# Performance work log

Measured on AMD Instinct MI355X. Metric: run time of the kernel, lower is better.

Reference implementation:

```python
import jax, jax.numpy as jnp
import numpy as np

B, S, H = 4, 2048, 1024
NH, HD = 16, 64
FF = 4096
EPS = 1e-5

def _ln(x, g, b):
    m = jnp.mean(x, axis=-1, keepdims=True)
    v = jnp.var(x, axis=-1, keepdims=True)
    return (x - m) * jax.lax.rsqrt(v + EPS) * g + b

def setup_inputs() -> dict:
    key = jax.random.key(0)
    ks = jax.random.split(key, 12)
    sc = 0.02
    return {
        "hidden_states": jax.random.normal(ks[0], (B, S, H), jnp.float32),
        "Wq": jax.random.normal(ks[1], (H, H), jnp.float32) * sc,
        "bq": jnp.zeros((H,), jnp.float32),
        "Wk": jax.random.normal(ks[2], (H, H), jnp.float32) * sc,
        "bk": jnp.zeros((H,), jnp.float32),
        "Wv": jax.random.normal(ks[3], (H, H), jnp.float32) * sc,
        "bv": jnp.zeros((H,), jnp.float32),
        "Wi": jax.random.normal(ks[4], (H, FF), jnp.float32) * sc,
        "bi": jnp.zeros((FF,), jnp.float32),
        "Wo": jax.random.normal(ks[5], (FF, H), jnp.float32) * sc,
        "bo": jnp.zeros((H,), jnp.float32),
        "g1": jnp.ones((H,), jnp.float32),
        "b1": jnp.zeros((H,), jnp.float32),
        "g2": jnp.ones((H,), jnp.float32),
        "b2": jnp.zeros((H,), jnp.float32),
    }

def reference(hidden_states, Wq, bq, Wk, bk, Wv, bv, Wi, bi, Wo, bo, g1, b1, g2, b2):
    x = hidden_states
    # projections -> [B, NH, S, HD]
    def split(t):
        return t.reshape(B, S, NH, HD).transpose(0, 2, 1, 3)
    q = split(x @ Wq + bq)
    k = split(x @ Wk + bk)
    v = split(x @ Wv + bv)
    scores = jnp.einsum('bhqd,bhkd->bhqk', q, k) / jnp.sqrt(jnp.float32(HD))
    probs = jax.nn.softmax(scores, axis=-1)
    ctx = jnp.einsum('bhqk,bhkd->bhqd', probs, v)
    attn_out = ctx.transpose(0, 2, 1, 3).reshape(B, S, H)
    h = _ln(x + attn_out, g1, b1)
    ffn = jax.nn.gelu(h @ Wi + bi, approximate=False) @ Wo + bo
    return _ln(h + ffn, g2, b2)
```

## Files before the change

kernel.cpp:

```cpp
#include <hip/hip_runtime.h>

#define B_  4
#define S_  2048
#define H_  1024
#define NH_ 16
#define HD_ 64
#define FF_ 4096
#define M_  (B_*S_)

typedef __bf16 bf16x8 __attribute__((ext_vector_type(8)));
typedef float  f32x4  __attribute__((ext_vector_type(4)));
typedef unsigned short ushort8v __attribute__((ext_vector_type(8)));
typedef unsigned short ushort4v __attribute__((ext_vector_type(4)));

typedef __attribute__((address_space(1))) void GVOID;
typedef __attribute__((address_space(3))) void LVOID;

__device__ __forceinline__ void g2l16(const void* g, void* l) {
  __builtin_amdgcn_global_load_lds((GVOID*)g, (LVOID*)l, 16, 0, 0);
}

#define MFMA16(a, b, c) __builtin_amdgcn_mfma_f32_16x16x32_bf16(a, b, c, 0, 0, 0)

#if __has_builtin(__builtin_amdgcn_exp2f)
#define EXP2(x) __builtin_amdgcn_exp2f(x)
#else
#define EXP2(x) exp2f(x)
#endif

__device__ __forceinline__ unsigned short f2bf(float f) {
  unsigned int u = __float_as_uint(f);
  u += 0x7fffu + ((u >> 16) & 1u);
  return (unsigned short)(u >> 16);
}
__device__ __forceinline__ float bf2f(unsigned short h) {
  return __uint_as_float(((unsigned int)h) << 16);
}

__device__ __forceinline__ float gelu_fast(float v) {
  float y = 0.7978845608f * (v + 0.044715f * v * v * v);
  float e = EXP2(y * 2.8853900818f);
  float th = 1.0f - 2.0f / (e + 1.0f);
  return 0.5f * v * (1.0f + th);
}

__device__ __forceinline__ void xcd_swz(int& bx, int& by) {
  int gx = gridDim.x;
  int flat = by * gx + bx;
  int cpx = (gx * gridDim.y) >> 3;
  int swz = (flat & 7) * cpx + (flat >> 3);
  bx = swz % gx;
  by = swz / gx;
}

__device__ __forceinline__ void xcd_swzT(int& bx, int& by) {
  int gy = gridDim.y;
  int flat = bx * gy + by;
  int cpx = (gridDim.x * gy) >> 3;
  int swz = (flat & 7) * cpx + (flat >> 3);
  by = swz % gy;
  bx = swz / gy;
}

__global__ __launch_bounds__(256) void cast_f32_bf16(const float* __restrict__ in,
                                                     unsigned short* __restrict__ out,
                                                     int n4) {
  int i = blockIdx.x * 256 + threadIdx.x;
  if (i >= n4) return;
  float4 v = reinterpret_cast<const float4*>(in)[i];
  ushort4v o;
  o[0] = f2bf(v.x); o[1] = f2bf(v.y); o[2] = f2bf(v.z); o[3] = f2bf(v.w);
  reinterpret_cast<ushort4v*>(out)[i] = o;
}

__global__ __launch_bounds__(256) void prep_weights(const float* __restrict__ Wq,
                                                    const float* __restrict__ Wk,
                                                    const float* __restrict__ Wv,
                                                    const float* __restrict__ Wi,
                                                    const float* __restrict__ Wo,
                                                    unsigned short* __restrict__ WqkvT,
                                                    unsigned short* __restrict__ WiT,
                                                    unsigned short* __restrict__ WoT) {
  __shared__ float t[32][33];
  int id = blockIdx.x;
  const float* in; unsigned short* out; int R, C, bx, by;
  if (id < 3072) {
    int seg = id >> 10, rem = id & 1023;
    in = (seg == 0) ? Wq : (seg == 1) ? Wk : Wv;
    out = WqkvT + (size_t)seg * H_ * H_;
    R = H_; C = H_;
    bx = rem & 31; by = rem >> 5;
  } else if (id < 3072 + 4096) {
    int rem = id - 3072;
    in = Wi; out = WiT; R = H_; C = FF_;
    bx = rem & 127; by = rem >> 7;
  } else {
    int rem = id - 3072 - 4096;
    in = Wo; out = WoT; R = FF_; C = H_;
    bx = rem & 31; by = rem >> 5;
  }
  bx *= 32; by *= 32;
  const int tx = threadIdx.x & 31, ty = threadIdx.x >> 5;
#pragma unroll
  for (int i = 0; i < 32; i += 8)
    t[ty + i][tx] = in[(size_t)(by + ty + i) * C + bx + tx];
  __syncthreads();
#pragma unroll
  for (int i = 0; i < 32; i += 8)
    out[(size_t)(bx + ty + i) * R + by + tx] = f2bf(t[tx][ty + i]);
}

#define ALOAD(bufv, mf, ks)                                                      \
  *reinterpret_cast<const bf16x8*>((char*)As + (bufv)*32768 + wm*16384 +         \
      ((mf)*16 + lr)*128 + (((((ks)*4 + kg)) ^ (lr & 7)) * 16))
#define BLOAD(bufv, nf, ks)                                                      \
  *reinterpret_cast<const bf16x8*>((char*)Bs + (bufv)*32768 + bh*16384 +         \
      (brow0 + (nf)*16 + lr)*128 + (((((ks)*4 + kg)) ^ (lr & 7)) * 16))

#define W4 asm volatile("s_waitcnt vmcnt(4)" ::: "memory")
#define W0 asm volatile("s_waitcnt vmcnt(0)" ::: "memory")
#define WN ((void)0)

#define PH_MFMA(MF0)                                                             \
  __builtin_amdgcn_s_barrier();                                                  \
  asm volatile("s_waitcnt lgkmcnt(0)" ::: "memory");                             \
  __builtin_amdgcn_s_setprio(1);                                                 \
  _Pragma("unroll")                                                              \
  for (int nf = 0; nf < 4; ++nf) {                                               \
    acc[MF0][nf]     = MFMA16(a_[0][0], bfr[nf][0], acc[MF0][nf]);               \
    acc[MF0][nf]     = MFMA16(a_[0][1], bfr[nf][1], acc[MF0][nf]);               \
    acc[MF0 + 1][nf] = MFMA16(a_[1][0], bfr[nf][0], acc[MF0 + 1][nf]);           \
    acc[MF0 + 1][nf] = MFMA16(a_[1][1], bfr[nf][1], acc[MF0 + 1][nf]);           \
  }                                                                              \
  __builtin_amdgcn_s_setprio(0);

#define GEMM_TILE(bufL, STGA, STGB, WAITOP)                                      \
  {                                                                              \
    bf16x8 bfr[4][2];                                                            \
    bf16x8 a_[2][2];                                                             \
    _Pragma("unroll")                                                            \
    for (int nf = 0; nf < 4; ++nf) {                                             \
      bfr[nf][0] = BLOAD(bufL, nf, 0);                                           \
      bfr[nf][1] = BLOAD(bufL, nf, 1);                                           \
    }                                                                            \
    a_[0][0] = ALOAD(bufL, 0, 0); a_[0][1] = ALOAD(bufL, 0, 1);                  \
    a_[1][0] = ALOAD(bufL, 1, 0); a_[1][1] = ALOAD(bufL, 1, 1);                  \
    if (STGA) {                                                                  \
      g2l16(sA + kA,       ldsA + ((bufL) ^ 1) * 32768);                         \
      g2l16(sA + rkI + kA, ldsA + ((bufL) ^ 1) * 32768 + 8192);                  \
    }                                                                            \
    PH_MFMA(0)                                                                   \
    __builtin_amdgcn_s_barrier();                                                \
    a_[0][0] = ALOAD(bufL, 2, 0); a_[0][1] = ALOAD(bufL, 2, 1);                  \
    a_[1][0] = ALOAD(bufL, 3, 0); a_[1][1] = ALOAD(bufL, 3, 1);                  \
    if (STGA) {                                                                  \
      g2l16(sA + rhK + kA,       ldsA + ((bufL) ^ 1) * 32768 + 16384);           \
      g2l16(sA + rhK + rkI + kA, ldsA + ((bufL) ^ 1) * 32768 + 16384 + 8192);    \
    }                                                                            \
    PH_MFMA(2)                                                                   \
    __builtin_amdgcn_s_barrier();                                                \
    a_[0][0] = ALOAD(bufL, 4, 0); a_[0][1] = ALOAD(bufL, 4, 1);                  \
    a_[1][0] = ALOAD(bufL, 5, 0); a_[1][1] = ALOAD(bufL, 5, 1);                  \
    if (STGB) {                                                                  \
      g2l16(sB + kB,       ldsB + (bufL) * 32768);                               \
      g2l16(sB + rkI + kB, ldsB + (bufL) * 32768 + 8192);                        \
    }                                                                            \
    PH_MFMA(4)                                                                   \
    __builtin_amdgcn_s_barrier();                                                \
    a_[0][0] = ALOAD(bufL, 6, 0); a_[0][1] = ALOAD(bufL, 6, 1);                  \
    a_[1][0] = ALOAD(bufL, 7, 0); a_[1][1] = ALOAD(bufL, 7, 1);                  \
    if (STGB) {                                                                  \
      g2l16(sB + rhK + kB,       ldsB + (bufL) * 32768 + 16384);                 \
      g2l16(sB + rhK + rkI + kB, ldsB + (bufL) * 32768 + 16384 + 8192);          \
    }                                                                            \
    PH_MFMA(6)                                                                   \
    WAITOP;                                                                      \
    __builtin_amdgcn_s_barrier();                                                \
    kA += 64; kB += 64;                                                          \
  }

#define GEMM256_CORE(A_, Bt_, LDK_, NKT_, KOFF_)                                 \
  __shared__ unsigned short As[2][2][128 * 64];                                  \
  __shared__ unsigned short Bs[2][2][128 * 64];                                  \
  const int tid  = threadIdx.x;                                                  \
  const int wave = tid >> 6;                                                     \
  const int lane = tid & 63;                                                     \
  const int kg   = lane >> 4;                                                    \
  const int lr   = lane & 15;                                                    \
  const int wm   = wave >> 2;                                                    \
  const int wn   = wave & 3;                                                     \
  const int bh   = wn >> 1;                                                      \
  const int brow0 = (wn & 1) * 64;                                               \
  const int sr = lane >> 3;                                                      \
  const int sc = ((lane & 7) ^ sr) * 8;                                          \
  const unsigned short* sA = &A_[(size_t)(m0 + wave * 8 + sr) * LDK_ + KOFF_ + sc];  \
  const unsigned short* sB = &Bt_[(size_t)(n0 + wave * 8 + sr) * LDK_ + KOFF_ + sc]; \
  char* ldsA = (char*)&As[0][0][0] + wave * 1024;                                \
  char* ldsB = (char*)&Bs[0][0][0] + wave * 1024;                                \
  const size_t rkI = (size_t)64 * LDK_;                                          \
  const size_t rhK = (size_t)128 * LDK_;                                         \
  f32x4 acc[8][4] = {};                                                          \
  const int nkt = (NKT_);                                                        \
  size_t kA = 64, kB = 128;                                                      \
  g2l16(sA,             ldsA);                                                   \
  g2l16(sA + rkI,       ldsA + 8192);                                            \
  g2l16(sA + rhK,       ldsA + 16384);                                           \
  g2l16(sA + rhK + rkI, ldsA + 16384 + 8192);                                    \
  g2l16(sB,             ldsB);                                                   \
  g2l16(sB + rkI,       ldsB + 8192);                                            \
  g2l16(sB + rhK,       ldsB + 16384);                                           \
  g2l16(sB + rhK + rkI, ldsB + 16384 + 8192);                                    \
  g2l16(sB + 64,             ldsB + 32768);                                      \
  g2l16(sB + rkI + 64,       ldsB + 32768 + 8192);                               \
  g2l16(sB + rhK + 64,       ldsB + 32768 + 16384);                              \
  g2l16(sB + rhK + rkI + 64, ldsB + 32768 + 16384 + 8192);                       \
  W4;                                                                            \
  __builtin_amdgcn_s_barrier();                                                  \
  for (int c = 0; c < nkt - 2; c += 2) {        \
    GEMM_TILE(0, 1, 1, W4)                                                       \
    GEMM_TILE(1, 1, 1, W4)                                                       \
  }                                                                              \
  GEMM_TILE(0, 1, 0, W0)             \
  GEMM_TILE(1, 0, 0, WN)

template<int ACT, int SPLITK>
__global__ __launch_bounds__(512, 1) void gemm256_tn(const unsigned short* __restrict__ A,
                                                     const unsigned short* __restrict__ Bt,
                                                     const float* __restrict__ bias,
                                                     unsigned short* __restrict__ C,
                                                     int M, int N, int K) {
  int bx = blockIdx.x, by = blockIdx.y;
  xcd_swzT(bx, by);
  const int z = SPLITK ? blockIdx.z : 0;
  const int Klen = SPLITK ? (K / gridDim.z) : K;
  const int Koff = z * Klen;
  const float* biasEff = (z == 0) ? bias : nullptr;
  const int m0 = bx * 256;
  const int n0 = by * 256;
  GEMM256_CORE(A, Bt, K, Klen >> 6, Koff)

  unsigned short* Cz = C + (size_t)z * M * N;
#pragma unroll
  for (int mf = 0; mf < 8; ++mf) {
#pragma unroll
    for (int nf = 0; nf < 4; ++nf) {
      int col = n0 + wn * 64 + nf * 16 + lr;
      float bc = biasEff ? biasEff[col] : 0.0f;
#pragma unroll
      for (int r = 0; r < 4; ++r) {
        int row = m0 + wm * 128 + mf * 16 + kg * 4 + r;
        float v = acc[mf][nf][r] + bc;
        if (ACT == 1) v = gelu_fast(v);
        Cz[(size_t)row * N + col] = f2bf(v);
      }
    }
  }
}

__global__ __launch_bounds__(512, 1) void gemm256_qkv(const unsigned short* __restrict__ A,
                                                      const unsigned short* __restrict__ Bt,
                                                      const float* __restrict__ bq,
                                                      const float* __restrict__ bk,
                                                      const float* __restrict__ bv,
                                                      unsigned short* __restrict__ qb,
                                                      unsigned short* __restrict__ kb,
                                                      unsigned short* __restrict__ vt,
                                                      float qscale) {
  int bx = blockIdx.x, by = blockIdx.y;
  xcd_swzT(bx, by);
  const int m0 = bx * 256;
  const int n0 = by * 256;
  GEMM256_CORE(A, Bt, H_, H_ >> 6, 0)

#pragma unroll
  for (int mf = 0; mf < 8; ++mf) {
#pragma unroll
    for (int nf = 0; nf < 4; ++nf) {
      int colb = n0 + wn * 64 + nf * 16;
      int col  = colb + lr;
      int seg  = colb >> 10;
      int row0 = m0 + wm * 128 + mf * 16 + kg * 4;
      if (seg == 0) {
        float bc = bq[col];
#pragma unroll
        for (int r = 0; r < 4; ++r)
          qb[(size_t)(row0 + r) * H_ + col] = f2bf((acc[mf][nf][r] + bc) * qscale);
      } else if (seg == 1) {
        float bc = bk[col - 1024];
#pragma unroll
        for (int r = 0; r < 4; ++r)
          kb[(size_t)(row0 + r) * H_ + col - 1024] = f2bf(acc[mf][nf][r] + bc);
      } else {
        float bc = bv[col - 2048];
        ushort4v o;
#pragma unroll
        for (int r = 0; r < 4; ++r) o[r] = f2bf(acc[mf][nf][r] + bc);
        *reinterpret_cast<ushort4v*>(&vt[(size_t)(col - 2048) * M_ + row0]) = o;
      }
    }
  }
}

__global__ __launch_bounds__(512) void attn_fwd(const unsigned short* __restrict__ Q,
                                                const unsigned short* __restrict__ Kb,
                                                const unsigned short* __restrict__ VT,
                                                unsigned short* __restrict__ O) {
  __shared__ unsigned short Ks[2][64 * 64];
  __shared__ unsigned short Vs[2][64 * 64];
  __shared__ __bf16 Ps[8][32 * 64];

  const int tid  = threadIdx.x;
  const int wave = tid >> 6;
  const int lane = tid & 63;
  const int kg   = lane >> 4;
  const int lr   = lane & 15;
  int bx = blockIdx.x, by = blockIdx.y;
  xcd_swz(bx, by);
  const int b  = by >> 4;
  const int h  = by & 15;
  const size_t rowbase = (size_t)b * S_;
  const int hcol = h * 64;
  const int bcol0 = b * S_;
  const int q0 = bx * 256 + wave * 32;

  const int rT = wave * 8 + (lane >> 3);
  const int ce = ((lane & 7) * 8) ^ (((lane >> 3) & 7) << 3);
  const int fswz = (lr & 7) << 3;

  bf16x8 qf[2][2];
#pragma unroll
  for (int sub = 0; sub < 2; ++sub)
#pragma unroll
    for (int d = 0; d < 2; ++d)
      qf[sub][d] = *reinterpret_cast<const bf16x8*>(
          &Q[(rowbase + q0 + sub * 16 + lr) * H_ + hcol + d * 32 + kg * 8]);

  bf16x8 ones;
#pragma unroll
  for (int i = 0; i < 8; ++i) ones[i] = (__bf16)1.0f;

  const f32x4 cinit = {-8.0f, -8.0f, -8.0f, -8.0f};

  f32x4 ctx[2][4] = {};
  f32x4 lsum[2] = {};

  auto stage = [&](int kt, int buf) {
    g2l16(&Kb[(rowbase + kt * 64 + rT) * H_ + hcol + ce], &Ks[buf][wave * 512]);
    g2l16(&VT[(size_t)(hcol + rT) * M_ + bcol0 + kt * 64 + ce], &Vs[buf][wave * 512]);
  };

  stage(0, 0);
  __syncthreads();

  const int NT = S_ / 64;
#pragma unroll 2
  for (int kt = 0; kt < NT; ++kt) {
    const int cur = kt & 1;
    if (kt + 1 < NT) stage(kt + 1, cur ^ 1);

    f32x4 s0[4], s1[4];
    __builtin_amdgcn_s_setprio(1);
#pragma unroll
    for (int nf = 0; nf < 4; ++nf) {
      int row = nf * 16 + lr;
      bf16x8 kf0 = *reinterpret_cast<const bf16x8*>(&Ks[cur][row * 64 + ((kg * 8) ^ fswz)]);
      bf16x8 kf1 = *reinterpret_cast<const bf16x8*>(&Ks[cur][row * 64 + ((32 + kg * 8) ^ fswz)]);
      f32x4 z0 = cinit, z1 = cinit;
      z0 = MFMA16(qf[0][0], kf0, z0);
      z0 = MFMA16(qf[0][1], kf1, z0);
      z1 = MFMA16(qf[1][0], kf0, z1);
      z1 = MFMA16(qf[1][1], kf1, z1);
      s0[nf] = z0;
      s1[nf] = z1;
    }
    __builtin_amdgcn_s_setprio(0);

#pragma unroll
    for (int nf = 0; nf < 4; ++nf)
#pragma unroll
      for (int r = 0; r < 4; ++r) {
        int row = kg * 4 + r;
        Ps[wave][row * 64 + ((nf * 16 + lr) ^ ((row & 7) << 3))] =
            (__bf16)EXP2(s0[nf][r]);
        Ps[wave][(16 + row) * 64 + ((nf * 16 + lr) ^ ((row & 7) << 3))] =
            (__bf16)EXP2(s1[nf][r]);
      }
    bf16x8 p00 = *reinterpret_cast<const bf16x8*>(
        &Ps[wave][lr * 64 + ((kg ^ (lr & 7)) << 3)]);
    bf16x8 p01 = *reinterpret_cast<const bf16x8*>(
        &Ps[wave][lr * 64 + (((4 + kg) ^ (lr & 7)) << 3)]);
    bf16x8 p10 = *reinterpret_cast<const bf16x8*>(
        &Ps[wave][(16 + lr) * 64 + ((kg ^ (lr & 7)) << 3)]);
    bf16x8 p11 = *reinterpret_cast<const bf16x8*>(
        &Ps[wave][(16 + lr) * 64 + (((4 + kg) ^ (lr & 7)) << 3)]);

    __builtin_amdgcn_s_setprio(1);
#pragma unroll
    for (int df = 0; df < 4; ++df) {
      int row = df * 16 + lr;
      bf16x8 vf0 = *reinterpret_cast<const bf16x8*>(&Vs[cur][row * 64 + ((kg * 8) ^ fswz)]);
      bf16x8 vf1 = *reinterpret_cast<const bf16x8*>(&Vs[cur][row * 64 + ((32 + kg * 8) ^ fswz)]);
      ctx[0][df] = MFMA16(p00, vf0, ctx[0][df]);
      ctx[0][df] = MFMA16(p01, vf1, ctx[0][df]);
      ctx[1][df] = MFMA16(p10, vf0, ctx[1][df]);
      ctx[1][df] = MFMA16(p11, vf1, ctx[1][df]);
    }
    lsum[0] = MFMA16(p00, ones, lsum[0]);
    lsum[0] = MFMA16(p01, ones, lsum[0]);
    lsum[1] = MFMA16(p10, ones, lsum[1]);
    lsum[1] = MFMA16(p11, ones, lsum[1]);
    __builtin_amdgcn_s_setprio(0);

    __syncthreads();
  }

#pragma unroll
  for (int sub = 0; sub < 2; ++sub)
#pragma unroll
    for (int r = 0; r < 4; ++r) {
      float rl = 1.0f / lsum[sub][r];
#pragma unroll
      for (int df = 0; df < 4; ++df) {
        float v = ctx[sub][df][r] * rl;
        O[(rowbase + q0 + sub * 16 + kg * 4 + r) * H_ + hcol + df * 16 + lr] = f2bf(v);
      }
    }
}

__global__ __launch_bounds__(256) void add_ln_b(const float* __restrict__ X,
                                                const unsigned short* __restrict__ Y,
                                                const float* __restrict__ g,
                                                const float* __restrict__ beta,
                                                unsigned short* __restrict__ outB) {
  const int row = blockIdx.x;
  const int tid = threadIdx.x;
  const int wave = tid >> 6, lane = tid & 63;
  __shared__ float red[8];

  const size_t base = (size_t)row * H_ + tid * 4;
  float4 xv = *reinterpret_cast<const float4*>(&X[base]);
  ushort4v yv = *reinterpret_cast<const ushort4v*>(&Y[base]);
  float vals[4] = {xv.x + bf2f(yv[0]), xv.y + bf2f(yv[1]),
                   xv.z + bf2f(yv[2]), xv.w + bf2f(yv[3])};
  float s = 0.0f, s2 = 0.0f;
#pragma unroll
  for (int i = 0; i < 4; ++i) { s += vals[i]; s2 += vals[i] * vals[i]; }
#pragma unroll
  for (int off = 32; off; off >>= 1) { s += __shfl_xor(s, off); s2 += __shfl_xor(s2, off); }
  if (lane == 0) { red[wave * 2] = s; red[wave * 2 + 1] = s2; }
  __syncthreads();
  s  = red[0] + red[2] + red[4] + red[6];
  s2 = red[1] + red[3] + red[5] + red[7];
  float mean = s * (1.0f / H_);
  float var  = s2 * (1.0f / H_) - mean * mean;
  float rstd = rsqrtf(var + 1e-5f);

  float4 gv = *reinterpret_cast<const float4*>(&g[tid * 4]);
  float4 bv = *reinterpret_cast<const float4*>(&beta[tid * 4]);
  float gs[4] = {gv.x, gv.y, gv.z, gv.w};
  float bs[4] = {bv.x, bv.y, bv.z, bv.w};
  ushort4v ob;
#pragma unroll
  for (int i = 0; i < 4; ++i)
    ob[i] = f2bf((vals[i] - mean) * rstd * gs[i] + bs[i]);
  *reinterpret_cast<ushort4v*>(&outB[base]) = ob;
}

__global__ __launch_bounds__(256) void add_ln3(const unsigned short* __restrict__ X,
                                               const unsigned short* __restrict__ Y0,
                                               const unsigned short* __restrict__ Y1,
                                               const float* __restrict__ g,
                                               const float* __restrict__ beta,
                                               float* __restrict__ outF) {
  const int row = blockIdx.x;
  const int tid = threadIdx.x;
  const int wave = tid >> 6, lane = tid & 63;
  __shared__ float red[8];

  const size_t base = (size_t)row * H_ + tid * 4;
  ushort4v xv = *reinterpret_cast<const ushort4v*>(&X[base]);
  ushort4v y0 = *reinterpret_cast<const ushort4v*>(&Y0[base]);
  ushort4v y1 = *reinterpret_cast<const ushort4v*>(&Y1[base]);
  float vals[4];
#pragma unroll
  for (int i = 0; i < 4; ++i)
    vals[i] = bf2f(xv[i]) + bf2f(y0[i]) + bf2f(y1[i]);
  float s = 0.0f, s2 = 0.0f;
#pragma unroll
  for (int i = 0; i < 4; ++i) { s += vals[i]; s2 += vals[i] * vals[i]; }
#pragma unroll
  for (int off = 32; off; off >>= 1) { s += __shfl_xor(s, off); s2 += __shfl_xor(s2, off); }
  if (lane == 0) { red[wave * 2] = s; red[wave * 2 + 1] = s2; }
  __syncthreads();
  s  = red[0] + red[2] + red[4] + red[6];
  s2 = red[1] + red[3] + red[5] + red[7];
  float mean = s * (1.0f / H_);
  float var  = s2 * (1.0f / H_) - mean * mean;
  float rstd = rsqrtf(var + 1e-5f);

  float4 gv = *reinterpret_cast<const float4*>(&g[tid * 4]);
  float4 bv = *reinterpret_cast<const float4*>(&beta[tid * 4]);
  float4 of;
  of.x = (vals[0] - mean) * rstd * gv.x + bv.x;
  of.y = (vals[1] - mean) * rstd * gv.y + bv.y;
  of.z = (vals[2] - mean) * rstd * gv.z + bv.z;
  of.w = (vals[3] - mean) * rstd * gv.w + bv.w;
  *reinterpret_cast<float4*>(&outF[base]) = of;
}

extern "C" void kernel_launch(void* const* d_in, const int* in_sizes, int n_in,
                              void* d_out, int out_size, void* d_ws, size_t ws_size,
                              hipStream_t stream) {
  const float* x  = (const float*)d_in[0];
  const float* Wq = (const float*)d_in[1];
  const float* bq = (const float*)d_in[2];
  const float* Wk = (const float*)d_in[3];
  const float* bk = (const float*)d_in[4];
  const float* Wv = (const float*)d_in[5];
  const float* bv = (const float*)d_in[6];
  const float* Wi = (const float*)d_in[7];
  const float* bi = (const float*)d_in[8];
  const float* Wo = (const float*)d_in[9];
  const float* bo = (const float*)d_in[10];
  const float* g1 = (const float*)d_in[11];
  const float* b1 = (const float*)d_in[12];
  const float* g2 = (const float*)d_in[13];
  const float* b2 = (const float*)d_in[14];

  unsigned char* ws = (unsigned char*)d_ws;
  size_t off = 0;
  auto alloc = [&](size_t bytes) { size_t o = off; off += (bytes + 255) & ~(size_t)255; return o; };

  unsigned short* WqkvT = (unsigned short*)(ws + alloc((size_t)3 * H_ * H_ * 2));
  unsigned short* WiT   = (unsigned short*)(ws + alloc((size_t)H_ * FF_ * 2));
  unsigned short* WoT   = (unsigned short*)(ws + alloc((size_t)FF_ * H_ * 2));
  unsigned short* hb    = (unsigned short*)(ws + alloc((size_t)M_ * H_ * 2));
  unsigned short* f1    = (unsigned short*)(ws + alloc((size_t)M_ * FF_ * 2));
  unsigned short* xb    = (unsigned short*)(ws + alloc((size_t)M_ * H_ * 2));
  unsigned short* qb    = (unsigned short*)(ws + alloc((size_t)M_ * H_ * 2));
  unsigned short* kb    = (unsigned short*)(ws + alloc((size_t)M_ * H_ * 2));
  unsigned short* vt    = (unsigned short*)(ws + alloc((size_t)M_ * H_ * 2));
  unsigned short* ao    = (unsigned short*)(ws + alloc((size_t)M_ * H_ * 2));
  unsigned short* f2p   = xb;

  {
    int n4 = (int)((size_t)M_ * H_ / 4);
    cast_f32_bf16<<<(n4 + 255) / 256, 256, 0, stream>>>(x, xb, n4);
  }
  prep_weights<<<3072 + 4096 + 4096, 256, 0, stream>>>(Wq, Wk, Wv, Wi, Wo,
                                                       WqkvT, WiT, WoT);

  const float QSCALE = 0.125f * 1.44269504088896340736f;

  gemm256_qkv<<<dim3(M_ / 256, 3072 / 256), 512, 0, stream>>>(xb, WqkvT, bq, bk, bv,
                                                              qb, kb, vt, QSCALE);

  attn_fwd<<<dim3(S_ / 256, B_ * NH_), 512, 0, stream>>>(qb, kb, vt, ao);

  add_ln_b<<<M_, 256, 0, stream>>>(x, ao, g1, b1, hb);

  gemm256_tn<1, 0><<<dim3(M_ / 256, FF_ / 256), 512, 0, stream>>>(hb, WiT, bi, f1, M_, FF_, H_);
  gemm256_tn<0, 1><<<dim3(M_ / 256, H_ / 256, 2), 512, 0, stream>>>(f1, WoT, bo, f2p, M_, H_, FF_);

  add_ln3<<<M_, 256, 0, stream>>>(hb, f2p, f2p + (size_t)M_ * H_, g2, b2, (float*)d_out);
}
```

Before: 394.9 us.

## Triple-buffer K/V tiles in attention with partial vmcnt waits

Moves the attention kernel's K/V shared-memory staging from double to triple buffering. Each tile now prefetches two tiles ahead and waits only on the older loads (vmcnt(2)) before a raw barrier, instead of a full __syncthreads. The loop is unrolled by three with a hand-written two-tile epilogue. This lets global loads overlap more compute, at the cost of extra LDS per block and correctness that depends on the exact load counts and tile indexing.

```diff
diff --git a/kernel.cpp b/kernel.cpp
--- a/kernel.cpp
+++ b/kernel.cpp
@@ -118,6 +118,7 @@
       (brow0 + (nf)*16 + lr)*128 + (((((ks)*4 + kg)) ^ (lr & 7)) * 16))
 
 #define W4 asm volatile("s_waitcnt vmcnt(4)" ::: "memory")
+#define W2 asm volatile("s_waitcnt vmcnt(2)" ::: "memory")
 #define W0 asm volatile("s_waitcnt vmcnt(0)" ::: "memory")
 #define WN ((void)0)
 
@@ -301,12 +302,72 @@
   }
 }
 
+#define ATTN_TILE(CUR, STGKT, STGBUF, DOSTG, WAITOP)                             \
+  {                                                                              \
+    if (DOSTG) stage((STGKT), (STGBUF));                                         \
+    f32x4 s0[4], s1[4];                                                          \
+    __builtin_amdgcn_s_setprio(1);                                               \
+    _Pragma("unroll")                                                            \
+    for (int nf = 0; nf < 4; ++nf) {                                             \
+      int row = nf * 16 + lr;                                                    \
+      bf16x8 kf0 = *reinterpret_cast<const bf16x8*>(                             \
+          &Ks[CUR][row * 64 + ((kg * 8) ^ fswz)]);                               \
+      bf16x8 kf1 = *reinterpret_cast<const bf16x8*>(                             \
+          &Ks[CUR][row * 64 + ((32 + kg * 8) ^ fswz)]);                          \
+      f32x4 z0 = cinit, z1 = cinit;                                              \
+      z0 = MFMA16(qf[0][0], kf0, z0);                                            \
+      z0 = MFMA16(qf[0][1], kf1, z0);                                            \
+      z1 = MFMA16(qf[1][0], kf0, z1);                                            \
+      z1 = MFMA16(qf[1][1], kf1, z1);                                            \
+      s0[nf] = z0; s1[nf] = z1;                                                  \
+    }                                                                            \
+    __builtin_amdgcn_s_setprio(0);                                               \
+    _Pragma("unroll")                                                            \
+    for (int nf = 0; nf < 4; ++nf)                                               \
+      _Pragma("unroll")                                                          \
+      for (int r = 0; r < 4; ++r) {                                              \
+        int row = kg * 4 + r;                                                    \
+        Ps[wave][row * 64 + ((nf * 16 + lr) ^ ((row & 7) << 3))] =               \
+            (__bf16)EXP2(s0[nf][r]);                                             \
+        Ps[wave][(16 + row) * 64 + ((nf * 16 + lr) ^ ((row & 7) << 3))] =        \
+            (__bf16)EXP2(s1[nf][r]);                                             \
+      }                                                                          \
+    bf16x8 p00 = *reinterpret_cast<const bf16x8*>(                               \
+        &Ps[wave][lr * 64 + ((kg ^ (lr & 7)) << 3)]);                            \
+    bf16x8 p01 = *reinterpret_cast<const bf16x8*>(                               \
+        &Ps[wave][lr * 64 + (((4 + kg) ^ (lr & 7)) << 3)]);                      \
+    bf16x8 p10 = *reinterpret_cast<const bf16x8*>(                               \
+        &Ps[wave][(16 + lr) * 64 + ((kg ^ (lr & 7)) << 3)]);                     \
+    bf16x8 p11 = *reinterpret_cast<const bf16x8*>(                               \
+        &Ps[wave][(16 + lr) * 64 + (((4 + kg) ^ (lr & 7)) << 3)]);               \
+    __builtin_amdgcn_s_setprio(1);                                               \
+    _Pragma("unroll")                                                            \
+    for (int df = 0; df < 4; ++df) {                                             \
+      int row = df * 16 + lr;                                                    \
+      bf16x8 vf0 = *reinterpret_cast<const bf16x8*>(                             \
+          &Vs[CUR][row * 64 + ((kg * 8) ^ fswz)]);                               \
+      bf16x8 vf1 = *reinterpret_cast<const bf16x8*>(                             \
+          &Vs[CUR][row * 64 + ((32 + kg * 8) ^ fswz)]);                          \
+      ctx[0][df] = MFMA16(p00, vf0, ctx[0][df]);                                 \
+      ctx[0][df] = MFMA16(p01, vf1, ctx[0][df]);                                 \
+      ctx[1][df] = MFMA16(p10, vf0, ctx[1][df]);                                 \
+      ctx[1][df] = MFMA16(p11, vf1, ctx[1][df]);                                 \
+    }                                                                            \
+    lsum[0] = MFMA16(p00, ones, lsum[0]);                                        \
+    lsum[0] = MFMA16(p01, ones, lsum[0]);                                        \
+    lsum[1] = MFMA16(p10, ones, lsum[1]);                                        \
+    lsum[1] = MFMA16(p11, ones, lsum[1]);                                        \
+    __builtin_amdgcn_s_setprio(0);                                               \
+    WAITOP;                                                                      \
+    __builtin_amdgcn_s_barrier();                                                \
+  }
+
 __global__ __launch_bounds__(512) void attn_fwd(const unsigned short* __restrict__ Q,
                                                 const unsigned short* __restrict__ Kb,
                                                 const unsigned short* __restrict__ VT,
                                                 unsigned short* __restrict__ O) {
-  __shared__ unsigned short Ks[2][64 * 64];
-  __shared__ unsigned short Vs[2][64 * 64];
+  __shared__ unsigned short Ks[3][64 * 64];
+  __shared__ unsigned short Vs[3][64 * 64];
   __shared__ __bf16 Ps[8][32 * 64];
 
   const int tid  = threadIdx.x;
@@ -350,69 +411,17 @@
   };
 
   stage(0, 0);
-  __syncthreads();
-
-  const int NT = S_ / 64;
-#pragma unroll 2
-  for (int kt = 0; kt < NT; ++kt) {
-    const int cur = kt & 1;
-    if (kt + 1 < NT) stage(kt + 1, cur ^ 1);
-
-    f32x4 s0[4], s1[4];
-    __builtin_amdgcn_s_setprio(1);
-#pragma unroll
-    for (int nf = 0; nf < 4; ++nf) {
-      int row = nf * 16 + lr;
-      bf16x8 kf0 = *reinterpret_cast<const bf16x8*>(&Ks[cur][row * 64 + ((kg * 8) ^ fswz)]);
-      bf16x8 kf1 = *reinterpret_cast<const bf16x8*>(&Ks[cur][row * 64 + ((32 + kg * 8) ^ fswz)]);
-      f32x4 z0 = cinit, z1 = cinit;
-      z0 = MFMA16(qf[0][0], kf0, z0);
-      z0 = MFMA16(qf[0][1], kf1, z0);
-      z1 = MFMA16(qf[1][0], kf0, z1);
-      z1 = MFMA16(qf[1][1], kf1, z1);
-      s0[nf] = z0;
-      s1[nf] = z1;
-    }
-    __builtin_amdgcn_s_setprio(0);
-
-#pragma unroll
-    for (int nf = 0; nf < 4; ++nf)
-#pragma unroll
-      for (int r = 0; r < 4; ++r) {
-        int row = kg * 4 + r;
-        Ps[wave][row * 64 + ((nf * 16 + lr) ^ ((row & 7) << 3))] =
-            (__bf16)EXP2(s0[nf][r]);
-        Ps[wave][(16 + row) * 64 + ((nf * 16 + lr) ^ ((row & 7) << 3))] =
-            (__bf16)EXP2(s1[nf][r]);
-      }
-    bf16x8 p00 = *reinterpret_cast<const bf16x8*>(
-        &Ps[wave][lr * 64 + ((kg ^ (lr & 7)) << 3)]);
-    bf16x8 p01 = *reinterpret_cast<const bf16x8*>(
-        &Ps[wave][lr * 64 + (((4 + kg) ^ (lr & 7)) << 3)]);
-    bf16x8 p10 = *reinterpret_cast<const bf16x8*>(
-        &Ps[wave][(16 + lr) * 64 + ((kg ^ (lr & 7)) << 3)]);
-    bf16x8 p11 = *reinterpret_cast<const bf16x8*>(
-        &Ps[wave][(16 + lr) * 64 + (((4 + kg) ^ (lr & 7)) << 3)]);
-
-    __builtin_amdgcn_s_setprio(1);
-#pragma unroll
-    for (int df = 0; df < 4; ++df) {
-      int row = df * 16 + lr;
-      bf16x8 vf0 = *reinterpret_cast<const bf16x8*>(&Vs[cur][row * 64 + ((kg * 8) ^ fswz)]);
-      bf16x8 vf1 = *reinterpret_cast<const bf16x8*>(&Vs[cur][row * 64 + ((32 + kg * 8) ^ fswz)]);
-      ctx[0][df] = MFMA16(p00, vf0, ctx[0][df]);
-      ctx[0][df] = MFMA16(p01, vf1, ctx[0][df]);
-      ctx[1][df] = MFMA16(p10, vf0, ctx[1][df]);
-      ctx[1][df] = MFMA16(p11, vf1, ctx[1][df]);
-    }
-    lsum[0] = MFMA16(p00, ones, lsum[0]);
-    lsum[0] = MFMA16(p01, ones, lsum[0]);
-    lsum[1] = MFMA16(p10, ones, lsum[1]);
-    lsum[1] = MFMA16(p11, ones, lsum[1]);
-    __builtin_amdgcn_s_setprio(0);
-
-    __syncthreads();
-  }
+  stage(1, 1);
+  W2;
+  __builtin_amdgcn_s_barrier();
+
+  for (int kt3 = 0; kt3 < 30; kt3 += 3) {
+    ATTN_TILE(0, kt3 + 2, 2, 1, W2)
+    ATTN_TILE(1, kt3 + 3, 0, 1, W2)
+    ATTN_TILE(2, kt3 + 4, 1, 1, W2)
+  }
+  ATTN_TILE(0, 0, 0, 0, W0)
+  ATTN_TILE(1, 0, 0, 0, WN)
 
 #pragma unroll
   for (int sub = 0; sub < 2; ++sub)
```

New measurement: 395.7 us. About the same (+0.2%).
